# Optimization experiments

Hardware: AMD Instinct MI355X
Metric: run time of the kernel (lower is better)

Reference implementation:

```python
import jax, jax.numpy as jnp
import numpy as np

B, H, W, N, DIM = 2, 64, 64, 4, 128
HEADS = 4
SPLIT = 2          # split_size; idx == 0 -> window = (H, SPLIT)
HEAD_DIM = DIM // HEADS
SCALE = HEAD_DIM ** -0.5


def setup_inputs() -> dict:
    key = jax.random.key(0)
    k1, k2, k3, k4 = jax.random.split(key, 4)
    query = jax.random.normal(k1, (B, H, W, N, DIM), jnp.float32)
    key_t = jax.random.normal(k2, (B, H, W, N, DIM), jnp.float32)
    value = jax.random.normal(k3, (B, H, W, N, DIM), jnp.float32)
    conv_w = jax.random.normal(k4, (DIM, 1, 3, 3), jnp.float32) * 0.1  # depthwise get_v
    return {"query": query, "key": key_t, "value": value, "conv_w": conv_w}


def _im2cswin(x, hs, ws, heads):
    # b (i hs) (j ws) n (h d) -> (b i j) h (hs ws n) d
    b, ht, wd, n, c = x.shape
    i, j = ht // hs, wd // ws
    d = c // heads
    x = x.reshape(b, i, hs, j, ws, n, heads, d)
    x = x.transpose(0, 1, 3, 6, 2, 4, 5, 7)  # b i j h hs ws n d
    return x.reshape(b * i * j, heads, hs * ws * n, d)


def _cswin_forward(query, key, value, conv_w):
    b, ht, wd, n, c = query.shape
    hs, ws = ht, SPLIT  # idx == 0; ht % hs == 0 and wd % ws == 0 -> no padding
    i, j = ht // hs, wd // ws
    Bw = b * i * j

    q = _im2cswin(query, hs, ws, HEADS) * SCALE
    k = _im2cswin(key, hs, ws, HEADS)

    # --- get_rpe (locally-enhanced positional encoding on value) ---
    # value windows: b i j n c hs ws
    vw = value.reshape(b, i, hs, j, ws, n, c).transpose(0, 1, 3, 5, 6, 2, 4)
    vw = vw.reshape(Bw, n, c, hs, ws)
    vimg = vw.reshape(Bw * n, c, hs, ws)
    conv = jax.lax.conv_general_dilated(
        vimg, conv_w, window_strides=(1, 1), padding=((1, 1), (1, 1)),
        dimension_numbers=("NCHW", "OIHW", "NCHW"), feature_group_count=c)
    conv = conv.reshape(Bw, n, c, hs, ws)
    rpe = conv.sum(axis=1, keepdims=True)  # Bw 1 c hs ws
    # subtract center-tap contribution of all other candidates at same pixel
    mask_n = (1.0 - jnp.eye(n, dtype=query.dtype)) * -1.0  # (n, n)
    center = conv_w[:, 0, 1, 1]  # (c,)
    tmp = vw * center[None, None, :, None, None]
    tmp = jnp.einsum("jk,bkdhw->bjdhw", mask_n, tmp)
    rpe = rpe + tmp  # Bw n c hs ws

    def to_tokens(t):
        # b n (h d) hs ws -> b h (hs ws n) d
        t = t.reshape(Bw, n, HEADS, HEAD_DIM, hs, ws)
        t = t.transpose(0, 2, 4, 5, 1, 3)
        return t.reshape(Bw, HEADS, hs * ws * n, HEAD_DIM)

    rpe = to_tokens(rpe)
    v = to_tokens(vw)

    # --- window attention mask: block self-edges between candidates at same pixel ---
    L = hs * ws * n
    tok = jnp.arange(L)
    sp = tok // n  # spatial index of each token
    amask = jnp.where(sp[:, None] == sp[None, :], -jnp.inf, 0.0)
    amask = jnp.where(tok[:, None] == tok[None, :], 0.0, amask).astype(query.dtype)

    attn = jnp.einsum("bhic,bhjc->bhij", q, k) + amask[None, None]
    attn = jax.nn.softmax(attn, axis=-1)
    x = jnp.einsum("bhij,bhjc->bhic", attn, v) + rpe

    # (b i j) h (hs ws n) d -> b (i hs) (j ws) n (h d)
    x = x.reshape(b, i, j, HEADS, hs, ws, n, HEAD_DIM)
    x = x.transpose(0, 1, 4, 2, 5, 6, 3, 7).reshape(b, ht, wd, n, c)
    return x


def reference(query, key, value, conv_w):
    return _cswin_forward(query, key, value, conv_w)
```

## Files before the change

kernel.cpp:

```cpp
#include <hip/hip_runtime.h>
#include <stdint.h>


typedef __bf16 bf16x8 __attribute__((ext_vector_type(8)));
typedef float f32x4 __attribute__((ext_vector_type(4)));

#if __has_builtin(__builtin_amdgcn_exp2f)
#define EXP2F __builtin_amdgcn_exp2f
#else
#define EXP2F exp2f
#endif

union U4 { uint4 u; bf16x8 v; unsigned short s[8]; };

__device__ __forceinline__ unsigned fbits(float f){ union{float f;unsigned u;}x; x.f=f; return x.u; }
__device__ __forceinline__ float bf2f(unsigned short h){ union{unsigned u;float f;}x; x.u=((unsigned)h)<<16; return x.f; }
__device__ __forceinline__ unsigned pk2f(float lo, float hi){
  return __builtin_amdgcn_perm(fbits(hi)+0x8000u, fbits(lo)+0x8000u, 0x07060302u);
}
__device__ __forceinline__ U4 pack8(float4 a, float4 b){
  U4 r;
  r.u.x = pk2f(a.x, a.y); r.u.y = pk2f(a.z, a.w);
  r.u.z = pk2f(b.x, b.y); r.u.w = pk2f(b.z, b.w);
  return r;
}

#define C_SCALE 0.25506953149031837f
#define M_SHIFT 20.0f

#define VT_OFF 0
#define S_OFF  33280
#define P_OFF  41984
#define LDS_BYTES 51200

__global__ __launch_bounds__(256, 3) void cswin_attn_kernel(
    const float* __restrict__ qg,
    const float* __restrict__ kg,
    const float* __restrict__ vg,
    const float* __restrict__ cwg,
    float* __restrict__ outg)
{
  __shared__ __align__(16) unsigned char smem[LDS_BYTES];
  unsigned short* VT = (unsigned short*)(smem + VT_OFF);
  const int tid = threadIdx.x;
  const int lane = tid & 63;
  const int wave = tid >> 6;
  const int qd = lane >> 4;
  const int n  = lane & 15;
  unsigned short* PB = (unsigned short*)(smem + P_OFF + wave * 2304);

  const int bh = blockIdx.x & 255;
  const int q4 = blockIdx.x >> 8;
  const int head = bh & 3;
  const int bw = bh >> 2;
  const int b  = bw >> 5;
  const int jj = bw & 31;

  const size_t wbase = (size_t)b * 2097152 + (size_t)(jj * 2) * 512 + head * 32;

  {
    int l0 = tid * 2;
    size_t off = wbase + (size_t)(l0 >> 3) * 32768 + (size_t)((l0 >> 2) & 1) * 512 + (l0 & 3) * 128;
    const float* p0 = vg + off;
    unsigned u0[32], u1[32];
#pragma unroll
    for (int c = 0; c < 8; c++){
      float4 a = ((const float4*)p0)[c];
      u0[c*4+0]=fbits(a.x)+0x8000u; u0[c*4+1]=fbits(a.y)+0x8000u;
      u0[c*4+2]=fbits(a.z)+0x8000u; u0[c*4+3]=fbits(a.w)+0x8000u;
    }
#pragma unroll
    for (int c = 0; c < 8; c++){
      float4 a = ((const float4*)(p0 + 128))[c];
      u1[c*4+0]=fbits(a.x)+0x8000u; u1[c*4+1]=fbits(a.y)+0x8000u;
      u1[c*4+2]=fbits(a.z)+0x8000u; u1[c*4+3]=fbits(a.w)+0x8000u;
    }
#pragma unroll
    for (int d = 0; d < 32; d++)
      *(unsigned*)(smem + VT_OFF + d * 1040 + l0 * 2) =
          __builtin_amdgcn_perm(u1[d], u0[d], 0x07060302u);
  }
  __syncthreads();
  {
    int sp = tid >> 1, dbase = (tid & 1) * 16;
    float sv[16];
#pragma unroll
    for (int dd = 0; dd < 16; dd++){
      uint2 rr = *(const uint2*)(smem + VT_OFF + (dbase + dd) * 1040 + sp * 8);
      sv[dd] = bf2f((unsigned short)(rr.x & 0xffff)) + bf2f((unsigned short)(rr.x >> 16))
             + bf2f((unsigned short)(rr.y & 0xffff)) + bf2f((unsigned short)(rr.y >> 16));
    }
#pragma unroll
    for (int dd = 0; dd < 16; dd += 2)
      *(unsigned*)(smem + S_OFF + (sp * 34 + dbase + dd) * 2) = pk2f(sv[dd], sv[dd+1]);
  }
  __syncthreads();

  const size_t lane_base = wbase + (size_t)(n >> 3) * 32768 + (size_t)((n >> 2) & 1) * 512 +
                           (size_t)(n & 3) * 128 + qd * 8;

  const int row0  = q4 * 128 + wave * 32;
  const int tilea = row0 >> 4;
  const int cka   = tilea >> 2;
  const int ta    = tilea & 3;

  U4 bqa, bqb;
  {
    const float* qa = qg + lane_base + (size_t)tilea * 65536;
    const float* qb = qa + 65536;
    bqa = pack8(((const float4*)qa)[0], ((const float4*)qa)[1]);
    bqb = pack8(((const float4*)qb)[0], ((const float4*)qb)[1]);
  }

  f32x4 o0a={0,0,0,0}, o1a={0,0,0,0}, o0b={0,0,0,0}, o1b={0,0,0,0};
  float la = 0.f, lb = 0.f;

  float4 nxt[8];
#pragma unroll
  for (int t = 0; t < 4; t++){
    const float* kp = kg + lane_base + (size_t)t * 65536;
    nxt[2*t] = ((const float4*)kp)[0]; nxt[2*t+1] = ((const float4*)kp)[1];
  }

#pragma unroll 1
  for (int ck = 0; ck < 8; ck++){
    U4 ak[4];
#pragma unroll
    for (int t = 0; t < 4; t++) ak[t] = pack8(nxt[2*t], nxt[2*t+1]);
    if (ck < 7){
#pragma unroll
      for (int t = 0; t < 4; t++){
        const float* kp = kg + lane_base + (size_t)((ck + 1) * 4 + t) * 65536;
        nxt[2*t] = ((const float4*)kp)[0]; nxt[2*t+1] = ((const float4*)kp)[1];
      }
    }

    const f32x4 zero = {0.f,0.f,0.f,0.f};
    f32x4 sa[4], sb[4];
#pragma unroll
    for (int t = 0; t < 4; t++){
      sa[t] = __builtin_amdgcn_mfma_f32_16x16x32_bf16(ak[t].v, bqa.v, zero, 0, 0, 0);
      sb[t] = __builtin_amdgcn_mfma_f32_16x16x32_bf16(ak[t].v, bqb.v, zero, 0, 0, 0);
    }
    if (ck == cka){
      bool dq = (qd == (n >> 2));
#pragma unroll
      for (int r = 0; r < 4; r++)
        if (dq && r != (n & 3)){ sa[ta][r] = -1e30f; sb[ta+1][r] = -1e30f; }
    }

#pragma unroll
    for (int t = 0; t < 4; t++)
#pragma unroll
      for (int r = 0; r < 4; r++){
        float p = EXP2F(__builtin_fmaf(sa[t][r], C_SCALE, -M_SHIFT));
        sa[t][r] = p; la += p;
      }
#pragma unroll
    for (int t = 0; t < 4; t++)
#pragma unroll
      for (int r = 0; r < 4; r++){
        float p = EXP2F(__builtin_fmaf(sb[t][r], C_SCALE, -M_SHIFT));
        sb[t][r] = p; lb += p;
      }

    U4 bv00, bv01, bv10, bv11;
    bv00.u = *(const uint4*)(VT + n * 520 + ck * 64 + qd * 8);
    bv01.u = *(const uint4*)(VT + n * 520 + ck * 64 + 32 + qd * 8);
    bv10.u = *(const uint4*)(VT + (16 + n) * 520 + ck * 64 + qd * 8);
    bv11.u = *(const uint4*)(VT + (16 + n) * 520 + ck * 64 + 32 + qd * 8);

#pragma unroll
    for (int tl = 0; tl < 4; tl++){
      uint2 w2; w2.x = pk2f(sa[tl][0], sa[tl][1]); w2.y = pk2f(sa[tl][2], sa[tl][3]);
      *(uint2*)(PB + n * 72 + tl * 16 + qd * 4) = w2;
    }
    __builtin_amdgcn_wave_barrier();
    U4 apA0, apA1;
    apA0.u = *(const uint4*)(PB + n * 72 + qd * 8);
    apA1.u = *(const uint4*)(PB + n * 72 + 32 + qd * 8);
    __builtin_amdgcn_wave_barrier();
#pragma unroll
    for (int tl = 0; tl < 4; tl++){
      uint2 w2; w2.x = pk2f(sb[tl][0], sb[tl][1]); w2.y = pk2f(sb[tl][2], sb[tl][3]);
      *(uint2*)(PB + n * 72 + tl * 16 + qd * 4) = w2;
    }
    __builtin_amdgcn_wave_barrier();
    U4 apB0, apB1;
    apB0.u = *(const uint4*)(PB + n * 72 + qd * 8);
    apB1.u = *(const uint4*)(PB + n * 72 + 32 + qd * 8);
    __builtin_amdgcn_wave_barrier();

    o0a = __builtin_amdgcn_mfma_f32_16x16x32_bf16(apA0.v, bv00.v, o0a, 0, 0, 0);
    o0a = __builtin_amdgcn_mfma_f32_16x16x32_bf16(apA1.v, bv01.v, o0a, 0, 0, 0);
    o1a = __builtin_amdgcn_mfma_f32_16x16x32_bf16(apA0.v, bv10.v, o1a, 0, 0, 0);
    o1a = __builtin_amdgcn_mfma_f32_16x16x32_bf16(apA1.v, bv11.v, o1a, 0, 0, 0);
    o0b = __builtin_amdgcn_mfma_f32_16x16x32_bf16(apB0.v, bv00.v, o0b, 0, 0, 0);
    o0b = __builtin_amdgcn_mfma_f32_16x16x32_bf16(apB1.v, bv01.v, o0b, 0, 0, 0);
    o1b = __builtin_amdgcn_mfma_f32_16x16x32_bf16(apB0.v, bv10.v, o1b, 0, 0, 0);
    o1b = __builtin_amdgcn_mfma_f32_16x16x32_bf16(apB1.v, bv11.v, o1b, 0, 0, 0);
  }

  la += __shfl_xor(la, 16); la += __shfl_xor(la, 32);
  lb += __shfl_xor(lb, 16); lb += __shfl_xor(lb, 32);

  float w9[2][9];
#pragma unroll
  for (int nt = 0; nt < 2; nt++){
    int c = head * 32 + nt * 16 + n;
#pragma unroll
    for (int t9 = 0; t9 < 9; t9++) w9[nt][t9] = cwg[c * 9 + t9];
  }

  const float ila = 1.f / la, ilb = 1.f / lb;

#pragma unroll
  for (int mt = 0; mt < 2; mt++){
    const int m0 = row0 + mt * 16;
    const float ilv = mt ? ilb : ila;
    const f32x4 oo0 = mt ? o0b : o0a;
    const f32x4 oo1 = mt ? o1b : o1a;
    float il[4];
#pragma unroll
    for (int r = 0; r < 4; r++) il[r] = __shfl(ilv, qd * 4 + r);

    const int sp = (m0 >> 2) + qd;
    const int h_ = sp >> 1, w_ = sp & 1;
#pragma unroll
    for (int nt = 0; nt < 2; nt++){
      const int d = nt * 16 + n;
      float acc = 0.f;
#pragma unroll
      for (int dy = -1; dy <= 1; dy++){
        int h2 = h_ + dy;
        bool hv = (h2 >= 0) && (h2 <= 63);
#pragma unroll
        for (int wp = 0; wp < 2; wp++){
          bool valid = hv && !((dy == 0) && (wp == w_));
          int ti = (dy + 1) * 3 + 1 + wp - w_;
          int sidx = valid ? ((h2 * 2 + wp) * 34 + d) : 0;
          float sval = valid ? bf2f(((const unsigned short*)(smem + S_OFF))[sidx]) : 0.f;
          acc += (valid ? w9[nt][ti] : 0.f) * sval;
        }
      }
      const float cwgt = w9[nt][4];
      const f32x4 ov = nt ? oo1 : oo0;
#pragma unroll
      for (int r = 0; r < 4; r++){
        float vv = bf2f(VT[d * 520 + (m0 + qd * 4 + r)]);
        float res = ov[r] * il[r] + acc + cwgt * vv;
        size_t off = (size_t)b * 2097152 + (size_t)h_ * 32768 +
                     (size_t)(jj * 2 + w_) * 512 + (size_t)r * 128 + head * 32 + d;
        outg[off] = res;
      }
    }
  }
}

extern "C" void kernel_launch(void* const* d_in, const int* in_sizes, int n_in,
                              void* d_out, int out_size, void* d_ws, size_t ws_size,
                              hipStream_t stream) {
  (void)in_sizes; (void)n_in; (void)d_ws; (void)ws_size; (void)out_size;
  cswin_attn_kernel<<<dim3(1024), dim3(256), 0, stream>>>(
      (const float*)d_in[0], (const float*)d_in[1], (const float*)d_in[2],
      (const float*)d_in[3], (float*)d_out);
}
```

Measured before the change: 132.7 us.

## Swizzle LDS layouts, drop candidate-sum staging buffer, raise occupancy to four blocks

```diff
diff --git a/kernel.cpp b/kernel.cpp
--- a/kernel.cpp
+++ b/kernel.cpp
@@ -29,11 +29,10 @@
 #define M_SHIFT 20.0f
 
 #define VT_OFF 0
-#define S_OFF  33280
-#define P_OFF  41984
-#define LDS_BYTES 51200
-
-__global__ __launch_bounds__(256, 3) void cswin_attn_kernel(
+#define PB_OFF 32768
+#define LDS_BYTES 40960
+
+__global__ __launch_bounds__(256, 4) void cswin_attn_kernel(
     const float* __restrict__ qg,
     const float* __restrict__ kg,
     const float* __restrict__ vg,
@@ -41,13 +40,15 @@
     float* __restrict__ outg)
 {
   __shared__ __align__(16) unsigned char smem[LDS_BYTES];
-  unsigned short* VT = (unsigned short*)(smem + VT_OFF);
   const int tid = threadIdx.x;
   const int lane = tid & 63;
   const int wave = tid >> 6;
   const int qd = lane >> 4;
   const int n  = lane & 15;
-  unsigned short* PB = (unsigned short*)(smem + P_OFF + wave * 2304);
+
+  const int swn = (n & 7) << 2;
+  const int xb0 = ((4 * qd) ^ swn) << 2;
+  const int xb1 = xb0 ^ 64;
 
   const int bh = blockIdx.x & 255;
   const int q4 = blockIdx.x >> 8;
@@ -77,22 +78,8 @@
     }
 #pragma unroll
     for (int d = 0; d < 32; d++)
-      *(unsigned*)(smem + VT_OFF + d * 1040 + l0 * 2) =
+      *(unsigned*)(smem + VT_OFF + d * 1024 + ((tid ^ ((d & 7) << 2)) << 2)) =
           __builtin_amdgcn_perm(u1[d], u0[d], 0x07060302u);
-  }
-  __syncthreads();
-  {
-    int sp = tid >> 1, dbase = (tid & 1) * 16;
-    float sv[16];
-#pragma unroll
-    for (int dd = 0; dd < 16; dd++){
-      uint2 rr = *(const uint2*)(smem + VT_OFF + (dbase + dd) * 1040 + sp * 8);
-      sv[dd] = bf2f((unsigned short)(rr.x & 0xffff)) + bf2f((unsigned short)(rr.x >> 16))
-             + bf2f((unsigned short)(rr.y & 0xffff)) + bf2f((unsigned short)(rr.y >> 16));
-    }
-#pragma unroll
-    for (int dd = 0; dd < 16; dd += 2)
-      *(unsigned*)(smem + S_OFF + (sp * 34 + dbase + dd) * 2) = pk2f(sv[dd], sv[dd+1]);
   }
   __syncthreads();
 
@@ -115,6 +102,8 @@
   f32x4 o0a={0,0,0,0}, o1a={0,0,0,0}, o0b={0,0,0,0}, o1b={0,0,0,0};
   float la = 0.f, lb = 0.f;
 
+  unsigned char* PBb = smem + PB_OFF + wave * 2048 + n * 128;
+
   float4 nxt[8];
 #pragma unroll
   for (int t = 0; t < 4; t++){
@@ -164,31 +153,33 @@
         sb[t][r] = p; lb += p;
       }
 
+    const unsigned char* vr0 = smem + VT_OFF + n * 1024 + ck * 128;
+    const unsigned char* vr1 = vr0 + 16 * 1024;
     U4 bv00, bv01, bv10, bv11;
-    bv00.u = *(const uint4*)(VT + n * 520 + ck * 64 + qd * 8);
-    bv01.u = *(const uint4*)(VT + n * 520 + ck * 64 + 32 + qd * 8);
-    bv10.u = *(const uint4*)(VT + (16 + n) * 520 + ck * 64 + qd * 8);
-    bv11.u = *(const uint4*)(VT + (16 + n) * 520 + ck * 64 + 32 + qd * 8);
+    bv00.u = *(const uint4*)(vr0 + xb0);
+    bv01.u = *(const uint4*)(vr0 + xb1);
+    bv10.u = *(const uint4*)(vr1 + xb0);
+    bv11.u = *(const uint4*)(vr1 + xb1);
 
 #pragma unroll
     for (int tl = 0; tl < 4; tl++){
       uint2 w2; w2.x = pk2f(sa[tl][0], sa[tl][1]); w2.y = pk2f(sa[tl][2], sa[tl][3]);
-      *(uint2*)(PB + n * 72 + tl * 16 + qd * 4) = w2;
+      *(uint2*)(PBb + (((8 * tl + 2 * qd) ^ swn) << 2)) = w2;
     }
     __builtin_amdgcn_wave_barrier();
     U4 apA0, apA1;
-    apA0.u = *(const uint4*)(PB + n * 72 + qd * 8);
-    apA1.u = *(const uint4*)(PB + n * 72 + 32 + qd * 8);
+    apA0.u = *(const uint4*)(PBb + xb0);
+    apA1.u = *(const uint4*)(PBb + xb1);
     __builtin_amdgcn_wave_barrier();
 #pragma unroll
     for (int tl = 0; tl < 4; tl++){
       uint2 w2; w2.x = pk2f(sb[tl][0], sb[tl][1]); w2.y = pk2f(sb[tl][2], sb[tl][3]);
-      *(uint2*)(PB + n * 72 + tl * 16 + qd * 4) = w2;
+      *(uint2*)(PBb + (((8 * tl + 2 * qd) ^ swn) << 2)) = w2;
     }
     __builtin_amdgcn_wave_barrier();
     U4 apB0, apB1;
-    apB0.u = *(const uint4*)(PB + n * 72 + qd * 8);
-    apB1.u = *(const uint4*)(PB + n * 72 + 32 + qd * 8);
+    apB0.u = *(const uint4*)(PBb + xb0);
+    apB1.u = *(const uint4*)(PBb + xb1);
     __builtin_amdgcn_wave_barrier();
 
     o0a = __builtin_amdgcn_mfma_f32_16x16x32_bf16(apA0.v, bv00.v, o0a, 0, 0, 0);
@@ -201,16 +192,16 @@
     o1b = __builtin_amdgcn_mfma_f32_16x16x32_bf16(apB1.v, bv11.v, o1b, 0, 0, 0);
   }
 
+  float w9[2][9];
+#pragma unroll
+  for (int nt = 0; nt < 2; nt++){
+    int c = head * 32 + nt * 16 + n;
+#pragma unroll
+    for (int t9 = 0; t9 < 9; t9++) w9[nt][t9] = cwg[c * 9 + t9];
+  }
+
   la += __shfl_xor(la, 16); la += __shfl_xor(la, 32);
   lb += __shfl_xor(lb, 16); lb += __shfl_xor(lb, 32);
-
-  float w9[2][9];
-#pragma unroll
-  for (int nt = 0; nt < 2; nt++){
-    int c = head * 32 + nt * 16 + n;
-#pragma unroll
-    for (int t9 = 0; t9 < 9; t9++) w9[nt][t9] = cwg[c * 9 + t9];
-  }
 
   const float ila = 1.f / la, ilb = 1.f / lb;
 
@@ -229,26 +220,32 @@
 #pragma unroll
     for (int nt = 0; nt < 2; nt++){
       const int d = nt * 16 + n;
+      const unsigned char* VTd = smem + VT_OFF + d * 1024;
       float acc = 0.f;
 #pragma unroll
       for (int dy = -1; dy <= 1; dy++){
         int h2 = h_ + dy;
         bool hv = (h2 >= 0) && (h2 <= 63);
+        int h2c = hv ? h2 : h_;
 #pragma unroll
         for (int wp = 0; wp < 2; wp++){
           bool valid = hv && !((dy == 0) && (wp == w_));
           int ti = (dy + 1) * 3 + 1 + wp - w_;
-          int sidx = valid ? ((h2 * 2 + wp) * 34 + d) : 0;
-          float sval = valid ? bf2f(((const unsigned short*)(smem + S_OFF))[sidx]) : 0.f;
-          acc += (valid ? w9[nt][ti] : 0.f) * sval;
+          int spn = h2c * 2 + wp;
+          uint2 sv = *(const uint2*)(VTd + (((2 * spn) ^ swn) << 2));
+          float s = bf2f((unsigned short)(sv.x & 0xffff)) + bf2f((unsigned short)(sv.x >> 16))
+                  + bf2f((unsigned short)(sv.y & 0xffff)) + bf2f((unsigned short)(sv.y >> 16));
+          acc += (valid ? w9[nt][ti] : 0.f) * s;
         }
       }
       const float cwgt = w9[nt][4];
       const f32x4 ov = nt ? oo1 : oo0;
+      uint2 vv4 = *(const uint2*)(VTd + ((((m0 >> 1) + 2 * qd) ^ swn) << 2));
+      float vf[4] = { bf2f((unsigned short)(vv4.x & 0xffff)), bf2f((unsigned short)(vv4.x >> 16)),
+                      bf2f((unsigned short)(vv4.y & 0xffff)), bf2f((unsigned short)(vv4.y >> 16)) };
 #pragma unroll
       for (int r = 0; r < 4; r++){
-        float vv = bf2f(VT[d * 520 + (m0 + qd * 4 + r)]);
-        float res = ov[r] * il[r] + acc + cwgt * vv;
+        float res = ov[r] * il[r] + acc + cwgt * vf[r];
         size_t off = (size_t)b * 2097152 + (size_t)h_ * 32768 +
                      (size_t)(jj * 2 + w_) * 512 + (size_t)r * 128 + head * 32 + d;
         outg[off] = res;
```

New measurement: 144.0 us. 8.6% more time.
